# Optimization experiments

Hardware: AMD Instinct MI355X
Metric: run time of the kernel (lower is better)

## Reference

```python
import jax, jax.numpy as jnp
import numpy as np

P = 9    # patch_size (number of shifts per axis)
DP = 1   # dilation_patch (pixel step per shift)


def setup_inputs() -> dict:
    key = jax.random.key(0)
    k1, k2 = jax.random.split(key)
    input1 = jax.random.normal(k1, (4, 256, 96, 128), dtype=jnp.float32)
    input2 = jax.random.normal(k2, (4, 256, 96, 128), dtype=jnp.float32)
    return {"input1": input1, "input2": input2}


def _correlation(input1, input2):
    # Faithful to iter_spatial_correlation_sample with kernel_size=1, stride=1,
    # padding=0, dilation=1: offsets are integer pixel shifts, and bilinear
    # grid_sample (align_corners=True, zeros outside) at integer coordinates is
    # exactly a zero-padded integer shift of input2.
    b, c, h, w = input2.shape
    off = DP * ((P - 1) // 2)  # center offset in pixels
    pad2 = jnp.pad(input2, ((0, 0), (0, 0), (off, off), (off, off)))
    rows = []
    for i in range(P):          # small fixed loop over patch offsets (81 total)
        cols = []
        for j in range(P):
            # window = input2 shifted by (dy, dx) = (i*DP - off, j*DP - off)
            win = jax.lax.dynamic_slice(pad2, (0, 0, i * DP, j * DP), (b, c, h, w))
            cols.append(jnp.einsum('bchw,bchw->bhw', input1, win))
        rows.append(jnp.stack(cols, axis=1))  # [b, P, h, w]
    return jnp.stack(rows, axis=1)            # [b, P, P, h, w]


def reference(input1, input2):
    return _correlation(input1, input2)
```

## Files before the change

### kernel.cpp

```cpp
#include <hip/hip_runtime.h>

#define CC 256
#define HH 96
#define WW 128
#define PP 9
#define OFF 4
#define PLANE (HH * WW)

#define HB 3
#define RN (HB + 8)
#define PX 32
#define SW 48
#define PAD 20
#define KCH 32
#define NCHK (CC / KCH)
#define TPB 384
#define DPAD 36
#define NU2 6
#define U2TOT (RN * 16 * 12)
#define ADVB (KCH * PLANE * 4)
#define PLB (PLANE * 4)
#define DSL (HB * SW * DPAD)

typedef _Float16 f16x8 __attribute__((ext_vector_type(8)));
typedef float fx4 __attribute__((ext_vector_type(4)));

union U16 { uint4 u; f16x8 h; };

__device__ __forceinline__ unsigned pk(float a, float b) {
#if __has_builtin(__builtin_amdgcn_cvt_pkrtz)
  auto r = __builtin_amdgcn_cvt_pkrtz(a, b);
  unsigned u; __builtin_memcpy(&u, &r, 4); return u;
#else
  _Float16 h0 = (_Float16)a, h1 = (_Float16)b;
  unsigned u = 0, v = 0; __builtin_memcpy(&u, &h0, 2); __builtin_memcpy(&v, &h1, 2);
  return u | (v << 16);
#endif
}

__global__ __launch_bounds__(TPB, 3) void corr_kernel(const float* __restrict__ in1,
                                                      const float* __restrict__ in2,
                                                      float* __restrict__ out) {
  __shared__ __align__(16) unsigned s2[RN][SW][PAD];
  __shared__ __align__(16) unsigned s1[HB][PX][PAD];

  const int bx = blockIdx.x;
  const int xcd = bx & 7;
  const int s = bx >> 3;
  const int xq = s & 3;
  const int t2 = s >> 2;
  const int b = t2 & 3;
  const int band = xcd * 4 + (t2 >> 2);
  const int h0 = band * HB;

  const int tid = threadIdx.x;
  const int wv = tid >> 6;
  const int wr = wv >> 1;
  const int wp = wv & 1;
  const int lane = tid & 63;
  const int ln = lane & 15;
  const int lg = lane >> 4;

  const char* in2p = (const char*)in2;
  const char* in1p = (const char*)in1;

  unsigned o2[NU2];
  unsigned vmask = 0;
#pragma unroll
  for (int k = 0; k < NU2; ++k) {
    const int u = tid + TPB * k;
    const bool inr = u < U2TOT;
    const int uu = inr ? u : tid;
    const int cp = uu & 15;
    const int qx = (uu >> 4) % 12;
    const int r = uu / 192;
    const int rg = h0 - OFF + r;
    const int gx = xq * PX - OFF + 4 * qx;
    const bool ok = inr && ((unsigned)rg < HH) && ((unsigned)gx <= WW - 4);
    const int rgc = rg < 0 ? 0 : (rg > HH - 1 ? HH - 1 : rg);
    const int gxc = gx < 0 ? 0 : (gx > WW - 4 ? WW - 4 : gx);
    o2[k] = (unsigned)(((b * CC + 2 * cp) * PLANE + rgc * WW + gxc) * 4);
    vmask |= (ok ? 1u : 0u) << k;
  }
  const int cp1 = tid & 15, qx1 = (tid >> 4) & 7, r1 = tid >> 7;
  unsigned o1 = (unsigned)(((b * CC + 2 * cp1) * PLANE + (h0 + r1) * WW + xq * PX + 4 * qx1) * 4);
  unsigned* const l1 = &s1[r1][4 * qx1][cp1];

  for (int i = tid; i < RN * SW * PAD; i += TPB) ((unsigned*)s2)[i] = 0u;

  fx4 acc[PP][2];
#pragma unroll
  for (int dy = 0; dy < PP; ++dy)
#pragma unroll
    for (int t = 0; t < 2; ++t) acc[dy][t] = (fx4)0.f;

  float4 fa[NU2], fb[NU2], ga, gb;

  auto ISSUE = [&]() {
#pragma unroll
    for (int k = 0; k < NU2; ++k) {
      fa[k] = *(const float4*)(in2p + o2[k]);
      fb[k] = *(const float4*)(in2p + o2[k] + PLB);
      o2[k] += ADVB;
    }
    ga = *(const float4*)(in1p + o1);
    gb = *(const float4*)(in1p + o1 + PLB);
    o1 += ADVB;
  };

  auto PKSTORE = [&]() {
#pragma unroll
    for (int k = 0; k < NU2; ++k) {
      if ((vmask >> k) & 1) {
        const int u = tid + TPB * k;
        const int cp = u & 15;
        const int qx = (u >> 4) % 12;
        const int r = u / 192;
        unsigned* base = &s2[r][4 * qx][cp];
        base[0 * PAD] = pk(fa[k].x, fb[k].x);
        base[1 * PAD] = pk(fa[k].y, fb[k].y);
        base[2 * PAD] = pk(fa[k].z, fb[k].z);
        base[3 * PAD] = pk(fa[k].w, fb[k].w);
      }
    }
    l1[0 * PAD] = pk(ga.x, gb.x);
    l1[1 * PAD] = pk(ga.y, gb.y);
    l1[2 * PAD] = pk(ga.z, gb.z);
    l1[3 * PAD] = pk(ga.w, gb.w);
  };

  auto COMPUTE = [&]() {
    U16 a; a.u = *(const uint4*)&s1[wr][wp * 16 + ln][4 * lg];
#pragma unroll
    for (int dy = 0; dy < PP; ++dy) {
#pragma unroll
      for (int t = 0; t < 2; ++t) {
        U16 bb; bb.u = *(const uint4*)&s2[wr + dy][wp * 16 + 16 * t + ln][4 * lg];
        acc[dy][t] = __builtin_amdgcn_mfma_f32_16x16x32_f16(a.h, bb.h, acc[dy][t], 0, 0, 0);
      }
    }
  };

  ISSUE();
  __syncthreads();
  PKSTORE();
  __syncthreads();

#pragma unroll 1
  for (int c = 0; c < NCHK; ++c) {
    if (c + 1 < NCHK) ISSUE();
    __builtin_amdgcn_sched_barrier(0);
    COMPUTE();
    __syncthreads();
    if (c + 1 < NCHK) {
      PKSTORE();
      __syncthreads();
    }
  }

  float* DL = (float*)&s2[0][0][0];
#pragma unroll
  for (int d0 = 0; d0 < PP; d0 += 2) {
    const int nd = (d0 + 1 < PP) ? 2 : 1;
#pragma unroll
    for (int sl = 0; sl < 2; ++sl) {
      if (sl < nd) {
#pragma unroll
        for (int t = 0; t < 2; ++t) {
          const int p2 = wp * 16 + 16 * t + ln;
          *(fx4*)&DL[sl * DSL + (wr * SW + p2) * DPAD + wp * 16 + 4 * lg] = acc[d0 + sl][t];
        }
      }
    }
    __syncthreads();
    const int tot = nd * HB * PP * PX;
    for (int id = tid; id < tot; id += TPB) {
      int slice = 0, rem = id;
      if (rem >= HB * PP * PX) { slice = 1; rem -= HB * PP * PX; }
      const int px = rem & 31;
      const int v = rem >> 5;
      const int dx = v % PP;
      const int rr = v / PP;
      out[(size_t)((b * PP + d0 + slice) * PP + dx) * PLANE + (size_t)(h0 + rr) * WW + xq * PX + px] =
          DL[slice * DSL + (rr * SW + px + dx) * DPAD + px];
    }
    __syncthreads();
  }
}

extern "C" void kernel_launch(void* const* d_in, const int* in_sizes, int n_in,
                              void* d_out, int out_size, void* d_ws, size_t ws_size,
                              hipStream_t stream) {
  const float* in1 = (const float*)d_in[0];
  const float* in2 = (const float*)d_in[1];
  float* out = (float*)d_out;
  corr_kernel<<<dim3(512), dim3(TPB), 0, stream>>>(in1, in2, out);
}
```

Measured before the change: 168.3 us.

## Remap global loads to per-pixel scalar loads with 8-channel vector LDS stores

After: 168.1 us. No clear change (-0.1%).

```diff
diff --git a/kernel.cpp b/kernel.cpp
--- a/kernel.cpp
+++ b/kernel.cpp
@@ -16,11 +16,10 @@
 #define NCHK (CC / KCH)
 #define TPB 384
 #define DPAD 36
+#define DSL (HB * SW * DPAD)
 #define NU2 6
-#define U2TOT (RN * 16 * 12)
 #define ADVB (KCH * PLANE * 4)
 #define PLB (PLANE * 4)
-#define DSL (HB * SW * DPAD)
 
 typedef _Float16 f16x8 __attribute__((ext_vector_type(8)));
 typedef float fx4 __attribute__((ext_vector_type(4)));
@@ -64,27 +63,28 @@
   const char* in2p = (const char*)in2;
   const char* in1p = (const char*)in1;
 
+  const int spx = tid % 48;
+  const int sq = tid / 48;
+  const int scb = sq & 3;
+  const int sr0 = sq >> 2;
+  const int gx2 = xq * PX - OFF + spx;
+  const bool okx = (unsigned)gx2 < WW;
+
   unsigned o2[NU2];
   unsigned vmask = 0;
 #pragma unroll
   for (int k = 0; k < NU2; ++k) {
-    const int u = tid + TPB * k;
-    const bool inr = u < U2TOT;
-    const int uu = inr ? u : tid;
-    const int cp = uu & 15;
-    const int qx = (uu >> 4) % 12;
-    const int r = uu / 192;
+    const int r = sr0 + 2 * k;
     const int rg = h0 - OFF + r;
-    const int gx = xq * PX - OFF + 4 * qx;
-    const bool ok = inr && ((unsigned)rg < HH) && ((unsigned)gx <= WW - 4);
-    const int rgc = rg < 0 ? 0 : (rg > HH - 1 ? HH - 1 : rg);
-    const int gxc = gx < 0 ? 0 : (gx > WW - 4 ? WW - 4 : gx);
-    o2[k] = (unsigned)(((b * CC + 2 * cp) * PLANE + rgc * WW + gxc) * 4);
+    const bool ok = (r < RN) && okx && ((unsigned)rg < HH);
+    o2[k] = ok ? (unsigned)(((b * CC + scb * 8) * PLANE + rg * WW + gx2) * 4) : 0u;
     vmask |= (ok ? 1u : 0u) << k;
   }
-  const int cp1 = tid & 15, qx1 = (tid >> 4) & 7, r1 = tid >> 7;
-  unsigned o1 = (unsigned)(((b * CC + 2 * cp1) * PLANE + (h0 + r1) * WW + xq * PX + 4 * qx1) * 4);
-  unsigned* const l1 = &s1[r1][4 * qx1][cp1];
+  const int tpx = tid & 31;
+  const int tq = tid >> 5;
+  const int tcb = tq & 3;
+  const int tr = tq >> 2;
+  const unsigned o1 = (unsigned)(((b * CC + tcb * 8) * PLANE + (h0 + tr) * WW + xq * PX + tpx) * 4);
 
   for (int i = tid; i < RN * SW * PAD; i += TPB) ((unsigned*)s2)[i] = 0u;
 
@@ -94,39 +94,39 @@
 #pragma unroll
     for (int t = 0; t < 2; ++t) acc[dy][t] = (fx4)0.f;
 
-  float4 fa[NU2], fb[NU2], ga, gb;
+  float f[NU2][8], g[8];
 
-  auto ISSUE = [&]() {
+  auto ISSUE = [&](unsigned cadv) {
 #pragma unroll
-    for (int k = 0; k < NU2; ++k) {
-      fa[k] = *(const float4*)(in2p + o2[k]);
-      fb[k] = *(const float4*)(in2p + o2[k] + PLB);
-      o2[k] += ADVB;
+    for (int k = 0; k < NU2; ++k)
+      if ((vmask >> k) & 1) {
+        const float* p = (const float*)(in2p + (o2[k] + cadv));
+#pragma unroll
+        for (int i = 0; i < 8; ++i) f[k][i] = p[i * PLANE];
+      }
+    {
+      const float* p = (const float*)(in1p + (o1 + cadv));
+#pragma unroll
+      for (int i = 0; i < 8; ++i) g[i] = p[i * PLANE];
     }
-    ga = *(const float4*)(in1p + o1);
-    gb = *(const float4*)(in1p + o1 + PLB);
-    o1 += ADVB;
   };
 
   auto PKSTORE = [&]() {
 #pragma unroll
-    for (int k = 0; k < NU2; ++k) {
+    for (int k = 0; k < NU2; ++k)
       if ((vmask >> k) & 1) {
-        const int u = tid + TPB * k;
-        const int cp = u & 15;
-        const int qx = (u >> 4) % 12;
-        const int r = u / 192;
-        unsigned* base = &s2[r][4 * qx][cp];
-        base[0 * PAD] = pk(fa[k].x, fb[k].x);
-        base[1 * PAD] = pk(fa[k].y, fb[k].y);
-        base[2 * PAD] = pk(fa[k].z, fb[k].z);
-        base[3 * PAD] = pk(fa[k].w, fb[k].w);
+        const int r = sr0 + 2 * k;
+        uint4 w;
+        w.x = pk(f[k][0], f[k][1]); w.y = pk(f[k][2], f[k][3]);
+        w.z = pk(f[k][4], f[k][5]); w.w = pk(f[k][6], f[k][7]);
+        *(uint4*)&s2[r][spx][4 * scb] = w;
       }
+    {
+      uint4 w;
+      w.x = pk(g[0], g[1]); w.y = pk(g[2], g[3]);
+      w.z = pk(g[4], g[5]); w.w = pk(g[6], g[7]);
+      *(uint4*)&s1[tr][tpx][4 * tcb] = w;
     }
-    l1[0 * PAD] = pk(ga.x, gb.x);
-    l1[1 * PAD] = pk(ga.y, gb.y);
-    l1[2 * PAD] = pk(ga.z, gb.z);
-    l1[3 * PAD] = pk(ga.w, gb.w);
   };
 
   auto COMPUTE = [&]() {
@@ -141,14 +141,14 @@
     }
   };
 
-  ISSUE();
+  ISSUE(0u);
   __syncthreads();
   PKSTORE();
   __syncthreads();
 
 #pragma unroll 1
   for (int c = 0; c < NCHK; ++c) {
-    if (c + 1 < NCHK) ISSUE();
+    if (c + 1 < NCHK) ISSUE((unsigned)(c + 1) * ADVB);
     __builtin_amdgcn_sched_barrier(0);
     COMPUTE();
     __syncthreads();
```
